# Kernel tuning notes

Hardware: AMD Instinct MI355X
Metric: run time of the kernel (lower is better)

## Reference

```python
import jax, jax.numpy as jnp
import numpy as np

B, T, C, H = 4, 2048, 1024, 16
D = C // H  # head dim = 64


def _layernorm(x, g, b, eps=1e-5):
    mu = jnp.mean(x, axis=-1, keepdims=True)
    var = jnp.var(x, axis=-1, keepdims=True)
    return (x - mu) * jax.lax.rsqrt(var + eps) * g + b


def setup_inputs() -> dict:
    key = jax.random.key(0)
    ks = jax.random.split(key, 8)
    s = 0.02
    return {
        "x": jax.random.normal(ks[0], (B, T, C), dtype=jnp.float32),
        "ln1_g": jnp.ones((C,), jnp.float32),
        "ln1_b": jnp.zeros((C,), jnp.float32),
        "W_qkv": jax.random.normal(ks[1], (C, 3 * C), dtype=jnp.float32) * s,
        "b_qkv": jnp.zeros((3 * C,), jnp.float32),
        "W_o": jax.random.normal(ks[2], (C, C), dtype=jnp.float32) * s,
        "b_o": jnp.zeros((C,), jnp.float32),
        "ln2_g": jnp.ones((C,), jnp.float32),
        "ln2_b": jnp.zeros((C,), jnp.float32),
        "W_fc": jax.random.normal(ks[3], (C, 4 * C), dtype=jnp.float32) * s,
        "b_fc": jnp.zeros((4 * C,), jnp.float32),
        "W_pr": jax.random.normal(ks[4], (4 * C, C), dtype=jnp.float32) * s,
        "b_pr": jnp.zeros((C,), jnp.float32),
    }


def reference(x, ln1_g, ln1_b, W_qkv, b_qkv, W_o, b_o, ln2_g, ln2_b, W_fc, b_fc, W_pr, b_pr):
    # --- attention sub-block ---
    h = _layernorm(x, ln1_g, ln1_b)
    qkv = h @ W_qkv + b_qkv                       # [B,T,3C]
    q, k, v = jnp.split(qkv, 3, axis=-1)
    q = q.reshape(B, T, H, D).transpose(0, 2, 1, 3)  # [B,H,T,D]
    k = k.reshape(B, T, H, D).transpose(0, 2, 1, 3)
    v = v.reshape(B, T, H, D).transpose(0, 2, 1, 3)
    att = jnp.einsum("bhqd,bhkd->bhqk", q, k) * (1.0 / jnp.sqrt(jnp.float32(D)))
    causal = jnp.tril(jnp.ones((T, T), dtype=bool))
    att = jnp.where(causal, att, jnp.float32(-jnp.inf))
    att = jax.nn.softmax(att, axis=-1)
    y = jnp.einsum("bhqk,bhkd->bhqd", att, v)     # [B,H,T,D]
    y = y.transpose(0, 2, 1, 3).reshape(B, T, C)
    y = y @ W_o + b_o
    x = x + y
    # --- FFN sub-block ---
    h2 = _layernorm(x, ln2_g, ln2_b)
    f = jax.nn.gelu(h2 @ W_fc + b_fc, approximate=False)  # nn.GELU default = exact
    f = f @ W_pr + b_pr
    return x + f
```

## Files before the change

### kernel.cpp

```cpp
#include <hip/hip_runtime.h>
#include <math.h>
#include <stdint.h>

#define Bz 4
#define Tz 2048
#define Cz 1024
#define Hz 16
#define Dz 64
#define MTOK (Bz*Tz)
#define ATT_SC 0.18033688011112042f

typedef __attribute__((ext_vector_type(8))) short short8;
typedef __attribute__((ext_vector_type(4))) short short4v;
typedef __attribute__((ext_vector_type(4))) float f32x4;

typedef unsigned int u32_g __attribute__((address_space(1)));
typedef unsigned int u32_l __attribute__((address_space(3)));

__device__ __forceinline__ unsigned short f2bf(float f) {
    unsigned int u = __float_as_uint(f);
    u += 0x7fffu + ((u >> 16) & 1u);
    return (unsigned short)(u >> 16);
}
__device__ __forceinline__ float bf2f(unsigned short h) {
    return __uint_as_float((unsigned int)h << 16);
}

__device__ __forceinline__ void async_cp16(const unsigned short* g, unsigned short* l) {
    __builtin_amdgcn_global_load_lds((const u32_g*)g, (u32_l*)l, 16, 0, 0);
}

#define BARX() asm volatile("s_barrier" ::: "memory")
#define VMCM(n) asm volatile("s_waitcnt vmcnt(" #n ")" ::: "memory")
#define LGKMC(n) do { asm volatile("s_waitcnt lgkmcnt(" #n ")" ::: "memory"); \
                      __builtin_amdgcn_sched_barrier(0); } while (0)

__global__ void transpose_wf(const float* __restrict__ W, unsigned short* __restrict__ Bf,
                             int K, int N) {
    const int nf = blockIdx.x;
    const int k0 = blockIdx.y * 128;
    const int tid = threadIdx.x;
    const int ktl = tid >> 6, lane = tid & 63;
    const int col = nf * 16 + (lane & 15);
    const int kk = k0 + ktl * 32 + (lane >> 4) * 8;
    const int KT = K >> 5;
    short8 o;
    #pragma unroll
    for (int j = 0; j < 8; j++)
        o[j] = (short)f2bf(W[(size_t)(kk + j) * N + col]);
    *(short8*)&Bf[(((size_t)nf * KT + (k0 >> 5) + ktl) * 64 + lane) * 8] = o;
}

__global__ void transpose_v(const unsigned short* __restrict__ in, unsigned short* __restrict__ out) {
    __shared__ unsigned short tile[64][68];
    const int bh = blockIdx.x;
    const int t0 = blockIdx.y * 64;
    const int tid = threadIdx.x;
    const int r4 = tid >> 4;
    const int c4 = tid & 15;
    #pragma unroll
    for (int p = 0; p < 4; p++) {
        const int r = p * 16 + r4;
        *(short4v*)&tile[r][c4 * 4] =
            *(const short4v*)&in[((size_t)bh * Tz + t0 + r) * Dz + c4 * 4];
    }
    __syncthreads();
    #pragma unroll
    for (int p = 0; p < 4; p++) {
        const int d = p * 16 + r4;
        short4v o;
        #pragma unroll
        for (int j = 0; j < 4; j++) o[j] = tile[c4 * 4 + j][d];
        *(short4v*)&out[((size_t)bh * Dz + d) * Tz + t0 + c4 * 4] = o;
    }
}

__global__ void ln_kernel(const float* __restrict__ x, const float* __restrict__ g,
                          const float* __restrict__ bb, unsigned short* __restrict__ out) {
    int tok = blockIdx.x, tid = threadIdx.x;
    const float4 v = ((const float4*)(x + (size_t)tok * Cz))[tid];
    float s = v.x + v.y + v.z + v.w;
    float sq = v.x * v.x + v.y * v.y + v.z * v.z + v.w * v.w;
    #pragma unroll
    for (int m = 1; m < 64; m <<= 1) { s += __shfl_xor(s, m); sq += __shfl_xor(sq, m); }
    __shared__ float red[8];
    int lane = tid & 63, wid = tid >> 6;
    if (!lane) { red[wid] = s; red[4 + wid] = sq; }
    __syncthreads();
    s = red[0] + red[1] + red[2] + red[3];
    sq = red[4] + red[5] + red[6] + red[7];
    float mu = s * (1.0f / Cz);
    float var = sq * (1.0f / Cz) - mu * mu;
    float rs = rsqrtf(var + 1e-5f);
    float4 gv = ((const float4*)g)[tid];
    float4 bv = ((const float4*)bb)[tid];
    short4v o;
    o[0] = f2bf((v.x - mu) * rs * gv.x + bv.x);
    o[1] = f2bf((v.y - mu) * rs * gv.y + bv.y);
    o[2] = f2bf((v.z - mu) * rs * gv.z + bv.z);
    o[3] = f2bf((v.w - mu) * rs * gv.w + bv.w);
    *(short4v*)(out + (size_t)tok * Cz + tid * 4) = o;
}

#define MODE_QKV 0
#define MODE_RESID 1
#define MODE_GELU 2

template <int MODE>
__launch_bounds__(256)
__global__ void gemm_rp(const unsigned short* __restrict__ A, const unsigned short* __restrict__ Bf,
                        int K, int N, const float* __restrict__ bias,
                        float* __restrict__ outf, unsigned short* __restrict__ outb,
                        const float* __restrict__ resid,
                        unsigned short* __restrict__ qo, unsigned short* __restrict__ ko,
                        unsigned short* __restrict__ vo) {
    __shared__ __align__(16) unsigned short LDS[4 * 2048];
    const int tid = threadIdx.x;
    const int lane = tid & 63;
    const int gn = tid >> 6;
    const int quad = lane >> 4, l15 = lane & 15;
    const int id = blockIdx.x;
    const int rr = id >> 3;
    const int m0 = ((id & 7) * 16 + (rr & 15)) * 64;
    const int n0 = (rr >> 4) * 256;
    const int NT = K >> 5;
    const int KT = K >> 5;

    const int lseg = (tid & 3) ^ ((tid >> 3) & 3);
    const int srow = tid >> 2;
    const unsigned short* Ag0 = A + (size_t)(m0 + srow) * K + lseg * 8;

    const unsigned ldsA = (unsigned)(uintptr_t)(u32_l*)LDS;
    unsigned offAb[4];
    #pragma unroll
    for (int mi = 0; mi < 4; mi++) {
        const int ra = mi * 16 + l15;
        offAb[mi] = (unsigned)(ra * 64 + ((quad ^ ((ra >> 1) & 3)) << 4));
    }

    const int nfg = (n0 >> 4) + gn * 4;
    const unsigned short* Bp[4];
    #pragma unroll
    for (int ni = 0; ni < 4; ni++)
        Bp[ni] = Bf + ((size_t)(nfg + ni) * KT) * 512 + lane * 8;

    f32x4 acc[4][4] = {};
    short8 afP[4], afQ[4], bfP[4], bfQ[4];

#define GLBa(bfX) do { _Pragma("unroll") for (int ni = 0; ni < 4; ni++) { \
    asm volatile("global_load_dwordx4 %0, %1, off" \
        : "=&v"(bfX[ni]) : "v"((unsigned long long)(uintptr_t)Bp[ni]) : "memory"); \
    Bp[ni] += 512; } } while (0)
#define STG(tt) async_cp16(Ag0 + (size_t)(tt) * 32, LDS + (((unsigned)(tt)) & 3u) * 2048 + tid * 8)
#define RDSa(afX, tt) do { \
    const unsigned sb_ = ldsA + (((unsigned)(tt)) & 3u) * 4096u; \
    _Pragma("unroll") for (int mi = 0; mi < 4; mi++) \
        asm volatile("ds_read_b128 %0, %1" : "=&v"(afX[mi]) : "v"(sb_ + offAb[mi])); } while (0)
#define MMS(afX, bfX) do { \
    __builtin_amdgcn_s_setprio(1); \
    _Pragma("unroll") for (int mi = 0; mi < 4; mi++) \
        _Pragma("unroll") for (int ni = 0; ni < 4; ni++) \
            acc[mi][ni] = __builtin_amdgcn_mfma_f32_16x16x32_bf16(afX[mi], bfX[ni], acc[mi][ni], 0, 0, 0); \
    __builtin_amdgcn_s_setprio(0); } while (0)

    STG(0); STG(1); GLBa(bfP); GLBa(bfQ); STG(2);
    VMCM(5);
    BARX();
    RDSa(afP, 0);

    for (int t = 0; t < NT; t += 2) {
        if (t + 3 < NT) STG(t + 3);
        RDSa(afQ, t + 1);
        LGKMC(4);
        MMS(afP, bfP);
        if (t + 2 < NT) GLBa(bfP);
        if (t + 3 < NT) { VMCM(5); } else { VMCM(0); }
        BARX();
        if (t + 4 < NT) STG(t + 4);
        if (t + 2 < NT) { RDSa(afP, t + 2); LGKMC(4); } else { LGKMC(0); }
        MMS(afQ, bfQ);
        if (t + 3 < NT) GLBa(bfQ);
        if (t + 4 < NT) { VMCM(5); } else { VMCM(0); }
        BARX();
    }
#undef GLBa
#undef STG
#undef RDSa
#undef MMS

    float bv[4];
    #pragma unroll
    for (int ni = 0; ni < 4; ni++) bv[ni] = bias[n0 + gn * 64 + ni * 16 + l15];

    if constexpr (MODE == MODE_QKV) {
        const int colb = n0 + gn * 64;
        const int which = colb >> 10;
        const int hh = (colb & 1023) >> 6;
        unsigned short* dst = (which == 0) ? qo : (which == 1) ? ko : vo;
        const float qsc = (which == 0) ? ATT_SC : 1.0f;
        #pragma unroll
        for (int mi = 0; mi < 4; mi++) {
            #pragma unroll
            for (int r = 0; r < 4; r++) {
                const int row = m0 + mi * 16 + quad * 4 + r;
                const int b_ = row >> 11, tt = row & 2047;
                unsigned short* rp = dst + ((size_t)(b_ * Hz + hh) * Tz + tt) * Dz;
                #pragma unroll
                for (int ni = 0; ni < 4; ni++)
                    rp[ni * 16 + l15] = f2bf((acc[mi][ni][r] + bv[ni]) * qsc);
            }
        }
    } else if constexpr (MODE == MODE_RESID) {
        #pragma unroll
        for (int mi = 0; mi < 4; mi++) {
            #pragma unroll
            for (int r = 0; r < 4; r++) {
                const int row = m0 + mi * 16 + quad * 4 + r;
                float* rp = outf + (size_t)row * N + n0 + gn * 64;
                const float* rr_ = resid + (size_t)row * N + n0 + gn * 64;
                #pragma unroll
                for (int ni = 0; ni < 4; ni++) {
                    const int c = ni * 16 + l15;
                    rp[c] = acc[mi][ni][r] + bv[ni] + rr_[c];
                }
            }
        }
    } else {
        #pragma unroll
        for (int mi = 0; mi < 4; mi++) {
            #pragma unroll
            for (int r = 0; r < 4; r++) {
                const int row = m0 + mi * 16 + quad * 4 + r;
                unsigned short* rp = outb + (size_t)row * N + n0 + gn * 64;
                #pragma unroll
                for (int ni = 0; ni < 4; ni++) {
                    float val = acc[mi][ni][r] + bv[ni];
                    float c = val * (1.0f + 0.044715f * val * val);
                    float e = __expf(1.5957691216057308f * c);
                    rp[ni * 16 + l15] = f2bf(val * e / (1.0f + e));
                }
            }
        }
    }
}

__launch_bounds__(256)
__global__ void attn_kernel(const unsigned short* __restrict__ qb, const unsigned short* __restrict__ kb,
                            const unsigned short* __restrict__ vt, unsigned short* __restrict__ y) {
    __shared__ __align__(16) unsigned short Klds[2][64 * 64];
    __shared__ __align__(16) unsigned short Vtl[2][64 * 64];
    __shared__ __align__(16) unsigned short Plds[4][16 * 72];
    const int tid = threadIdx.x;
    const int lane = tid & 63, wid = tid >> 6;
    const int quad = lane >> 4, l15 = lane & 15;
    const int bh = blockIdx.x & 63;
    const int qt = 15 - (int)(blockIdx.x >> 6);
    const size_t baseT = (size_t)bh * Tz;
    const size_t vbase = (size_t)bh * Dz;
    const int qb0 = qt * 128;

    const int srow = lane >> 3;
    const int swz = ((lane & 7) ^ srow) * 8;
    const unsigned short* kg0 = kb + (baseT + wid * 8 + srow) * Dz + swz;
    const unsigned short* kg1 = kg0 + (size_t)32 * Dz;
    const unsigned short* vg0 = vt + (vbase + wid * 8 + srow) * Tz + swz;
    const unsigned short* vg1 = vg0 + (size_t)32 * Tz;
    const int lofs = wid * 512 + lane * 8;

#define ASTG(ci_) do { const int s_ = (ci_) & 1; const int kk_ = (ci_) * 64; \
    async_cp16(kg0 + (size_t)kk_ * Dz, &Klds[s_][lofs]); \
    async_cp16(kg1 + (size_t)kk_ * Dz, &Klds[s_][2048 + lofs]); \
    async_cp16(vg0 + kk_, &Vtl[s_][lofs]); \
    async_cp16(vg1 + kk_, &Vtl[s_][2048 + lofs]); } while (0)

    ASTG(0);

    short8 qf[2][2];
    {
        const unsigned short* q0p = qb + (baseT + qb0 + wid * 16 + l15) * Dz + quad * 8;
        qf[0][0] = *(const short8*)q0p;
        qf[0][1] = *(const short8*)(q0p + 32);
        const unsigned short* q1p = q0p + (size_t)64 * Dz;
        qf[1][0] = *(const short8*)q1p;
        qf[1][1] = *(const short8*)(q1p + 32);
    }

    f32x4 o[2][4] = {};
    float lsum[2][4] = {{0.f,0.f,0.f,0.f},{0.f,0.f,0.f,0.f}};

    const int nchunk = 2 * qt + 2;

    for (int ci = 0; ci < nchunk; ci++) {
        VMCM(0);
        BARX();
        if (ci + 1 < nchunk) ASTG(ci + 1);
        const int sl = ci & 1;
        const int k0 = ci * 64;

        #pragma unroll
        for (int t = 0; t < 2; t++) {
            if (t == 0 && ci == nchunk - 1) continue;
            const bool diag = (ci == nchunk - 2 + t);

            f32x4 s[4];
            #pragma unroll
            for (int c = 0; c < 4; c++) {
                const int rk = c * 16 + l15;
                short8 kf0 = *(const short8*)&Klds[sl][rk * 64 + ((quad ^ (rk & 7)) * 8)];
                short8 kf1 = *(const short8*)&Klds[sl][rk * 64 + (((quad + 4) ^ (rk & 7)) * 8)];
                f32x4 z = {};
                z = __builtin_amdgcn_mfma_f32_16x16x32_bf16(qf[t][0], kf0, z, 0, 0, 0);
                s[c] = __builtin_amdgcn_mfma_f32_16x16x32_bf16(qf[t][1], kf1, z, 0, 0, 0);
            }
            const int qr = qb0 + t * 64 + wid * 16 + quad * 4;
            #pragma unroll
            for (int c = 0; c < 4; c++)
                #pragma unroll
                for (int r = 0; r < 4; r++) {
                    float p = exp2f(s[c][r]);
                    if (diag) {
                        int key = k0 + c * 16 + l15;
                        p = (key <= qr + r) ? p : 0.f;
                    }
                    s[c][r] = p;
                    lsum[t][r] += p;
                }
            unsigned short* P = Plds[wid];
            #pragma unroll
            for (int c = 0; c < 4; c++) {
                #pragma unroll
                for (int rp2 = 0; rp2 < 2; rp2++) {
                    unsigned pk;
                    asm("v_cvt_pk_bf16_f32 %0, %1, %2"
                        : "=v"(pk) : "v"(s[c][2 * rp2]), "v"(s[c][2 * rp2 + 1]));
                    P[(quad * 4 + 2 * rp2) * 72 + c * 16 + l15] = (unsigned short)pk;
                    P[(quad * 4 + 2 * rp2 + 1) * 72 + c * 16 + l15] = (unsigned short)(pk >> 16);
                }
            }
            short8 pf0 = *(const short8*)&P[l15 * 72 + quad * 8];
            short8 pf1 = *(const short8*)&P[l15 * 72 + 32 + quad * 8];
            #pragma unroll
            for (int nc = 0; nc < 4; nc++) {
                const int rv = nc * 16 + l15;
                short8 vf0 = *(const short8*)&Vtl[sl][rv * 64 + ((quad ^ (rv & 7)) * 8)];
                short8 vf1 = *(const short8*)&Vtl[sl][rv * 64 + (((quad + 4) ^ (rv & 7)) * 8)];
                o[t][nc] = __builtin_amdgcn_mfma_f32_16x16x32_bf16(pf0, vf0, o[t][nc], 0, 0, 0);
                o[t][nc] = __builtin_amdgcn_mfma_f32_16x16x32_bf16(pf1, vf1, o[t][nc], 0, 0, 0);
            }
        }
    }
#undef ASTG

    const int b_ = bh >> 4, hh = bh & 15;
    #pragma unroll
    for (int t = 0; t < 2; t++)
        #pragma unroll
        for (int r = 0; r < 4; r++) {
            float ls = lsum[t][r];
            #pragma unroll
            for (int m = 1; m < 16; m <<= 1) ls += __shfl_xor(ls, m);
            float inv = 1.0f / ls;
            size_t tok = (size_t)qb0 + t * 64 + wid * 16 + quad * 4 + r;
            unsigned short* yr = y + ((size_t)b_ * Tz + tok) * Cz + hh * Dz;
            #pragma unroll
            for (int nc = 0; nc < 4; nc++)
                yr[nc * 16 + l15] = f2bf(o[t][nc][r] * inv);
        }
}

extern "C" void kernel_launch(void* const* d_in, const int* in_sizes, int n_in,
                              void* d_out, int out_size, void* d_ws, size_t ws_size,
                              hipStream_t stream) {
    const float* x    = (const float*)d_in[0];
    const float* ln1g = (const float*)d_in[1];
    const float* ln1b = (const float*)d_in[2];
    const float* Wqkv = (const float*)d_in[3];
    const float* bqkv = (const float*)d_in[4];
    const float* Wo   = (const float*)d_in[5];
    const float* bo   = (const float*)d_in[6];
    const float* ln2g = (const float*)d_in[7];
    const float* ln2b = (const float*)d_in[8];
    const float* Wfc  = (const float*)d_in[9];
    const float* bfc  = (const float*)d_in[10];
    const float* Wpr  = (const float*)d_in[11];
    const float* bpr  = (const float*)d_in[12];
    float* out = (float*)d_out;

    char* ws = (char*)d_ws;
    size_t off = 0;
    auto alloc = [&](size_t bytes) { void* p = ws + off; off += (bytes + 255) & ~(size_t)255; return p; };
    unsigned short* wqkv_t = (unsigned short*)alloc((size_t)3072 * 1024 * 2);
    unsigned short* wo_t   = (unsigned short*)alloc((size_t)1024 * 1024 * 2);
    unsigned short* wfc_t  = (unsigned short*)alloc((size_t)4096 * 1024 * 2);
    unsigned short* wpr_t  = (unsigned short*)alloc((size_t)1024 * 4096 * 2);
    unsigned short* h1     = (unsigned short*)alloc((size_t)MTOK * Cz * 2);
    unsigned short* qbuf   = (unsigned short*)alloc((size_t)MTOK * Cz * 2);
    unsigned short* kbuf   = (unsigned short*)alloc((size_t)MTOK * Cz * 2);
    unsigned short* vbuf   = (unsigned short*)alloc((size_t)MTOK * Cz * 2);
    unsigned short* ybuf   = (unsigned short*)alloc((size_t)MTOK * Cz * 2);
    float*          x1     = (float*)alloc((size_t)MTOK * Cz * 4);
    unsigned short* h2     = (unsigned short*)alloc((size_t)MTOK * Cz * 2);
    unsigned short* fbuf   = (unsigned short*)alloc((size_t)MTOK * 4096 * 2);
    unsigned short* vtmp   = fbuf;

    transpose_wf<<<dim3(3072 / 16, 1024 / 128), 256, 0, stream>>>(Wqkv, wqkv_t, 1024, 3072);
    transpose_wf<<<dim3(1024 / 16, 1024 / 128), 256, 0, stream>>>(Wo, wo_t, 1024, 1024);
    transpose_wf<<<dim3(4096 / 16, 1024 / 128), 256, 0, stream>>>(Wfc, wfc_t, 1024, 4096);
    transpose_wf<<<dim3(1024 / 16, 4096 / 128), 256, 0, stream>>>(Wpr, wpr_t, 4096, 1024);

    ln_kernel<<<MTOK, 256, 0, stream>>>(x, ln1g, ln1b, h1);
    gemm_rp<MODE_QKV><<<1536, 256, 0, stream>>>(h1, wqkv_t, 1024, 3072, bqkv,
                                                nullptr, nullptr, nullptr, qbuf, kbuf, vtmp);
    transpose_v<<<dim3(64, 32), 256, 0, stream>>>(vtmp, vbuf);
    attn_kernel<<<1024, 256, 0, stream>>>(qbuf, kbuf, vbuf, ybuf);
    gemm_rp<MODE_RESID><<<512, 256, 0, stream>>>(ybuf, wo_t, 1024, 1024, bo,
                                                 x1, nullptr, x, nullptr, nullptr, nullptr);
    ln_kernel<<<MTOK, 256, 0, stream>>>(x1, ln2g, ln2b, h2);
    gemm_rp<MODE_GELU><<<2048, 256, 0, stream>>>(h2, wfc_t, 1024, 4096, bfc,
                                                 nullptr, fbuf, nullptr, nullptr, nullptr, nullptr);
    gemm_rp<MODE_RESID><<<512, 256, 0, stream>>>(fbuf, wpr_t, 4096, 1024, bpr,
                                                 out, nullptr, x1, nullptr, nullptr, nullptr);
}
```

Before: 504.1 us.

## Deepen GEMM K-step to 64 with double register fragments per stage

The GEMM main loop now processes 64 K-elements per pipeline stage instead of 32. Each stage stages two A sub-tiles into LDS and loads two sets of B fragments, and one barrier covers 32 MFMAs instead of 16. This halves the number of barriers and loop iterations and gives more work to overlap with memory latency. In exchange LDS doubles to 32 KB per block and register pressure rises, which may reduce occupancy. The waitcnt thresholds were rewritten for the new schedule.

New measurement: 485.5 us. 1.04x faster.

```diff
diff --git a/kernel.cpp b/kernel.cpp
--- a/kernel.cpp
+++ b/kernel.cpp
@@ -114,7 +114,7 @@
                         const float* __restrict__ resid,
                         unsigned short* __restrict__ qo, unsigned short* __restrict__ ko,
                         unsigned short* __restrict__ vo) {
-    __shared__ __align__(16) unsigned short LDS[4 * 2048];
+    __shared__ __align__(16) unsigned short LDS[4 * 4096];
     const int tid = threadIdx.x;
     const int lane = tid & 63;
     const int gn = tid >> 6;
@@ -123,7 +123,7 @@
     const int rr = id >> 3;
     const int m0 = ((id & 7) * 16 + (rr & 15)) * 64;
     const int n0 = (rr >> 4) * 256;
-    const int NT = K >> 5;
+    const int NT = K >> 6;
     const int KT = K >> 5;
 
     const int lseg = (tid & 3) ^ ((tid >> 3) & 3);
@@ -145,15 +145,19 @@
         Bp[ni] = Bf + ((size_t)(nfg + ni) * KT) * 512 + lane * 8;
 
     f32x4 acc[4][4] = {};
-    short8 afP[4], afQ[4], bfP[4], bfQ[4];
+    short8 afP0[4], afP1[4], afQ0[4], afQ1[4];
+    short8 bfP0[4], bfP1[4], bfQ0[4], bfQ1[4];
 
 #define GLBa(bfX) do { _Pragma("unroll") for (int ni = 0; ni < 4; ni++) { \
     asm volatile("global_load_dwordx4 %0, %1, off" \
         : "=&v"(bfX[ni]) : "v"((unsigned long long)(uintptr_t)Bp[ni]) : "memory"); \
     Bp[ni] += 512; } } while (0)
-#define STG(tt) async_cp16(Ag0 + (size_t)(tt) * 32, LDS + (((unsigned)(tt)) & 3u) * 2048 + tid * 8)
-#define RDSa(afX, tt) do { \
-    const unsigned sb_ = ldsA + (((unsigned)(tt)) & 3u) * 4096u; \
+#define STG(tt) do { unsigned short* sp_ = LDS + (((unsigned)(tt)) & 3u) * 4096; \
+    const size_t kof_ = (size_t)(tt) * 64; \
+    async_cp16(Ag0 + kof_, sp_ + tid * 8); \
+    async_cp16(Ag0 + kof_ + 32, sp_ + 2048 + tid * 8); } while (0)
+#define RDSa(afX, tt, ks) do { \
+    const unsigned sb_ = ldsA + (((unsigned)(tt)) & 3u) * 8192u + (ks) * 4096u; \
     _Pragma("unroll") for (int mi = 0; mi < 4; mi++) \
         asm volatile("ds_read_b128 %0, %1" : "=&v"(afX[mi]) : "v"(sb_ + offAb[mi])); } while (0)
 #define MMS(afX, bfX) do { \
@@ -163,30 +167,32 @@
             acc[mi][ni] = __builtin_amdgcn_mfma_f32_16x16x32_bf16(afX[mi], bfX[ni], acc[mi][ni], 0, 0, 0); \
     __builtin_amdgcn_s_setprio(0); } while (0)
 
-    STG(0); STG(1); GLBa(bfP); GLBa(bfQ); STG(2);
-    VMCM(5);
+#define BODY(tt, afC0, afC1, bfC0, bfC1, afN0, afN1, bfN0, bfN1) do { \
+    const bool hasS_ = (tt) + 3 < NT, hasB_ = (tt) + 1 < NT; \
+    if (hasS_) STG((tt) + 3); \
+    if (hasB_) { GLBa(bfN0); GLBa(bfN1); } \
+    if (hasS_ && hasB_) { VMCM(10); } else if (hasB_) { VMCM(8); } else { VMCM(0); } \
+    if (hasB_) { RDSa(afN0, (tt) + 1, 0); RDSa(afN1, (tt) + 1, 1); LGKMC(8); } \
+    else { LGKMC(0); } \
+    MMS(afC0, bfC0); \
+    MMS(afC1, bfC1); \
+    BARX(); } while (0)
+
+    STG(0); STG(1); STG(2);
+    GLBa(bfP0); GLBa(bfP1);
+    VMCM(8);
     BARX();
-    RDSa(afP, 0);
+    RDSa(afP0, 0, 0); RDSa(afP1, 0, 1);
 
     for (int t = 0; t < NT; t += 2) {
-        if (t + 3 < NT) STG(t + 3);
-        RDSa(afQ, t + 1);
-        LGKMC(4);
-        MMS(afP, bfP);
-        if (t + 2 < NT) GLBa(bfP);
-        if (t + 3 < NT) { VMCM(5); } else { VMCM(0); }
-        BARX();
-        if (t + 4 < NT) STG(t + 4);
-        if (t + 2 < NT) { RDSa(afP, t + 2); LGKMC(4); } else { LGKMC(0); }
-        MMS(afQ, bfQ);
-        if (t + 3 < NT) GLBa(bfQ);
-        if (t + 4 < NT) { VMCM(5); } else { VMCM(0); }
-        BARX();
+        BODY(t,     afP0, afP1, bfP0, bfP1, afQ0, afQ1, bfQ0, bfQ1);
+        BODY(t + 1, afQ0, afQ1, bfQ0, bfQ1, afP0, afP1, bfP0, bfP1);
     }
 #undef GLBa
 #undef STG
 #undef RDSa
 #undef MMS
+#undef BODY
 
     float bv[4];
     #pragma unroll
```
